# Kernel optimization log

Measured on AMD Instinct MI355X. Metric: run time of the kernel, lower is better.

Reference implementation:

```python
import jax, jax.numpy as jnp
import numpy as np

N_SUPPORT = 32768
N_QUERY = 16384
D = 512
K = 32
U = 128
NEG_BIG = -1e30  # masked-out attention logit; all-masked class -> uniform weights == mean fallback


def setup_inputs() -> dict:
    key = jax.random.key(0)
    k1, k2, k3, k4, k5 = jax.random.split(key, 5)
    query = jax.random.normal(k1, (N_QUERY, D), dtype=jnp.float32)
    support = jax.random.normal(k2, (N_SUPPORT, D), dtype=jnp.float32)
    labels = jax.random.randint(k3, (N_SUPPORT,), 0, K, dtype=jnp.int32)
    # Xavier-normal-ish init for per-class projection V (U,D) and attention vector w (U,1)
    V = jax.random.normal(k4, (K, U, D), dtype=jnp.float32) * np.float32(np.sqrt(2.0 / (U + D)))
    w = jax.random.normal(k5, (K, U), dtype=jnp.float32) * np.float32(np.sqrt(2.0 / (U + 1)))
    return {"query_embeddings": query, "support_embeddings": support,
            "support_labels": labels, "V": V, "w": w}


def reference(query_embeddings, support_embeddings, support_labels, V, w):
    # --- attention-weighted prototypes (vectorized over classes via masked softmax) ---
    # projected[k,n,u] = tanh(V[k] @ x_n)
    projected = jnp.tanh(jnp.einsum('nd,kud->knu', support_embeddings, V))
    attn_logits = jnp.einsum('knu,ku->kn', projected, w)              # (K, N)
    mask = support_labels[None, :] == jnp.arange(K, dtype=support_labels.dtype)[:, None]
    attn_logits = jnp.where(mask, attn_logits, NEG_BIG)
    # per-class softmax over support samples; an empty class yields uniform weights,
    # i.e. prototype = mean(embeddings) -- exactly the torch fallback branch.
    attn = jax.nn.softmax(attn_logits, axis=1)                        # (K, N)
    prototypes = jnp.einsum('kn,nd->kd', attn, support_embeddings)    # (K, D)

    # --- squared-euclidean distance classification ---
    q2 = jnp.sum(query_embeddings * query_embeddings, axis=1, keepdims=True)   # (B, 1)
    p2 = jnp.sum(prototypes * prototypes, axis=1)[None, :]                     # (1, K)
    dists = q2 + p2 - 2.0 * (query_embeddings @ prototypes.T)                  # (B, K)
    return jax.nn.log_softmax(-dists, axis=1)
```

## Files before the change

### kernel.cpp

```cpp
#include <hip/hip_runtime.h>
#include <hip/hip_bf16.h>

#define N_SUPPORT 32768
#define N_QUERY   16384
#define DIM       512
#define NCLS      32
#define NU        128
#define NBLK      (N_SUPPORT / 256)

#define OFF_IDX      0
#define OFF_COUNT    131072
#define OFF_START    131200
#define OFF_M        131456
#define OFF_Z        131584
#define OFF_P2       131712
#define OFF_LOGIT    132096
#define OFF_PRAW     263168
#define OFF_PROTO    328704
#define OFF_BHIST    394240
#define OFF_BOFFS    410624
#define OFF_VBF      458752
#define OFF_PBF      4653056

typedef __attribute__((ext_vector_type(8))) short short8;
typedef __attribute__((ext_vector_type(4))) short short4v;
typedef __attribute__((ext_vector_type(4))) float f32x4;

typedef __attribute__((address_space(3))) unsigned int lds_u32;
typedef const __attribute__((address_space(1))) unsigned int glb_u32;

__device__ inline unsigned short f2bf(float f) {
    unsigned int x = __builtin_bit_cast(unsigned int, f);
    unsigned int r = x + 0x7fffu + ((x >> 16) & 1u);
    return (unsigned short)(r >> 16);
}
__device__ inline float bf2f(unsigned short h) {
    unsigned int u = ((unsigned int)h) << 16;
    return __builtin_bit_cast(float, u);
}

__device__ inline short8 pack_bf8(float4 f0, float4 f1) {
    short8 pk;
    pk[0] = f2bf(f0.x); pk[1] = f2bf(f0.y); pk[2] = f2bf(f0.z); pk[3] = f2bf(f0.w);
    pk[4] = f2bf(f1.x); pk[5] = f2bf(f1.y); pk[6] = f2bf(f1.z); pk[7] = f2bf(f1.w);
    return pk;
}

__device__ inline void pack_hilo(float4 f0, float4 f1, short8& hi, short8& lo) {
    float v[8] = {f0.x, f0.y, f0.z, f0.w, f1.x, f1.y, f1.z, f1.w};
    #pragma unroll
    for (int i = 0; i < 8; i++) {
        unsigned short h = f2bf(v[i]);
        hi[i] = (short)h;
        lo[i] = (short)f2bf(v[i] - bf2f(h));
    }
}

__global__ void k_vcast(const float* __restrict__ V, short* __restrict__ Vbf,
                        float* __restrict__ praw, const int* __restrict__ labels,
                        int* __restrict__ bhist) {
    __shared__ int h[NCLS];
    int tid = threadIdx.x;
    bool dohist = (blockIdx.x < NBLK);
    if (dohist) {
        if (tid < NCLS) h[tid] = 0;
        __syncthreads();
        atomicAdd(&h[labels[blockIdx.x * 256 + tid]], 1);
    }
    int i = blockIdx.x * 256 + tid;
    int ob = i * 4;
    int j0  = ob & 7;
    int s   = (ob >> 3) & 7;
    int u   = (ob >> 6) & 127;
    int c   = (ob >> 13) & 7;
    int k   = ob >> 16;
    int d   = c * 64 + ((s ^ (u & 7)) * 8) + j0;
    float4 f = *(const float4*)(V + ((size_t)(k * 128 + u) * DIM + d));
    short4v o;
    o[0] = f2bf(f.x); o[1] = f2bf(f.y); o[2] = f2bf(f.z); o[3] = f2bf(f.w);
    *(short4v*)(Vbf + (size_t)ob) = o;
    if (i < (NCLS * DIM) / 4) *(float4*)(praw + i * 4) = make_float4(0.f, 0.f, 0.f, 0.f);
    if (dohist) {
        __syncthreads();
        if (tid < NCLS) bhist[blockIdx.x * NCLS + tid] = h[tid];
    }
}

__global__ void k_scan2(const int* __restrict__ bhist, int* __restrict__ boffs,
                        int* __restrict__ start, int* __restrict__ count) {
    __shared__ int tot[NCLS];
    int tid = threadIdx.x;
    if (tid < NCLS) {
        int s = 0;
        for (int b = 0; b < NBLK; b++) {
            boffs[b * NCLS + tid] = s;
            s += bhist[b * NCLS + tid];
        }
        tot[tid] = s;
    }
    __syncthreads();
    if (tid == 0) {
        int run = 0;
        for (int k = 0; k < NCLS; k++) {
            start[k] = run;
            count[k] = tot[k];
            run += tot[k];
        }
        start[NCLS] = run;
    }
}

__global__ void k_scatter(const int* __restrict__ labels, const int* __restrict__ boffs,
                          const int* __restrict__ start, int* __restrict__ idx_c) {
    __shared__ int whist[4][NCLS];
    int tid = threadIdx.x;
    int n = blockIdx.x * 256 + tid;
    int l = labels[n];
    int lane = tid & 63, wid = tid >> 6;
    unsigned long long mymask = 0ull;
    #pragma unroll
    for (int k = 0; k < NCLS; k++) {
        unsigned long long mk = __ballot(l == k);
        if (k == l) mymask = mk;
        if (lane == k) whist[wid][k] = __popcll(mk);
    }
    int rank = __popcll(mymask & ((1ull << lane) - 1ull));
    __syncthreads();
    int wbase = 0;
    for (int w = 0; w < wid; w++) wbase += whist[w][l];
    idx_c[start[l] + boffs[blockIdx.x * NCLS + l] + wbase + rank] = n;
}

__launch_bounds__(256, 1)
__global__ void k_logits(const float* __restrict__ support, const short* __restrict__ Vbf,
                         const float* __restrict__ w, const int* __restrict__ idx_c,
                         const int* __restrict__ start, const int* __restrict__ count,
                         float* __restrict__ logit_c) {
    int k = blockIdx.y;
    int cnt = count[k];
    int base = blockIdx.x * 32;
    if (base >= cnt) return;
    int M = min(32, cnt - base);
    int s0 = start[k] + base;
    int t = threadIdx.x;

    __shared__ __align__(16) short Xs[32 * 64];
    __shared__ __align__(16) short Vs[128 * 64];
    __shared__ float part[4][32];
    __shared__ int sidx[32];
    if (t < 32) sidx[t] = idx_c[s0 + ((t < M) ? t : 0)];
    __syncthreads();

    int l = t & 63, wv = t >> 6;
    int lo16 = l & 15, hi4 = l >> 4;

    int xrow = t >> 3, xslot = t & 7;
    int xdst = xrow * 64 + ((xslot ^ (xrow & 7)) * 8);
    const float* xsrc = support + (size_t)sidx[xrow] * DIM + xslot * 8;
    const short* Vkc = Vbf + (size_t)k * (8 * 128 * 64);

    f32x4 acc[2][2];
    #pragma unroll
    for (int mt = 0; mt < 2; mt++)
        #pragma unroll
        for (int nt = 0; nt < 2; nt++) acc[mt][nt] = (f32x4){0.f, 0.f, 0.f, 0.f};

    float4 xv0 = *(const float4*)(xsrc);
    float4 xv1 = *(const float4*)(xsrc + 4);

    for (int c = 0; c < 8; ++c) {
        __syncthreads();
        #pragma unroll
        for (int rep = 0; rep < 4; rep++) {
            int u = t + 256 * rep;
            __builtin_amdgcn_global_load_lds(
                (glb_u32*)(Vkc + (size_t)c * 8192 + (size_t)u * 8),
                (lds_u32*)&Vs[u * 8], 16, 0, 0);
        }
        *(short8*)&Xs[xdst] = pack_bf8(xv0, xv1);
        __syncthreads();
        if (c < 7) {
            xv0 = *(const float4*)(xsrc + (c + 1) * 64);
            xv1 = *(const float4*)(xsrc + (c + 1) * 64 + 4);
        }
        #pragma unroll
        for (int ks = 0; ks < 2; ks++) {
            short8 a[2], b[2];
            #pragma unroll
            for (int mt = 0; mt < 2; mt++) {
                int ar = mt * 16 + lo16;
                a[mt] = *(short8*)&Xs[ar * 64 + (((ks * 4 + hi4) ^ (ar & 7)) * 8)];
            }
            #pragma unroll
            for (int nt = 0; nt < 2; nt++) {
                int vr = wv * 32 + nt * 16 + lo16;
                b[nt] = *(short8*)&Vs[vr * 64 + (((ks * 4 + hi4) ^ (vr & 7)) * 8)];
            }
            #pragma unroll
            for (int mt = 0; mt < 2; mt++)
                #pragma unroll
                for (int nt = 0; nt < 2; nt++)
                    acc[mt][nt] = __builtin_amdgcn_mfma_f32_16x16x32_bf16(a[mt], b[nt], acc[mt][nt], 0, 0, 0);
        }
    }

    float w0 = w[k * NU + wv * 32 + lo16];
    float w1 = w[k * NU + wv * 32 + 16 + lo16];
    #pragma unroll
    for (int mt = 0; mt < 2; mt++) {
        #pragma unroll
        for (int r = 0; r < 4; r++) {
            float val = tanhf(acc[mt][0][r]) * w0 + tanhf(acc[mt][1][r]) * w1;
            val += __shfl_xor(val, 1);
            val += __shfl_xor(val, 2);
            val += __shfl_xor(val, 4);
            val += __shfl_xor(val, 8);
            if (lo16 == 0) part[wv][mt * 16 + hi4 * 4 + r] = val;
        }
    }
    __syncthreads();
    if (t < M) {
        logit_c[s0 + t] = part[0][t] + part[1][t] + part[2][t] + part[3][t];
    }
}

__global__ void k_mz(const float* __restrict__ logit_c, const int* __restrict__ start,
                     const int* __restrict__ count, float* __restrict__ m, float* __restrict__ Z) {
    int k = blockIdx.x;
    int cnt = count[k], s0 = start[k];
    int tid = threadIdx.x;
    __shared__ float red[256];
    float mx = -1e30f;
    for (int i = tid; i < cnt; i += 256) mx = fmaxf(mx, logit_c[s0 + i]);
    red[tid] = mx; __syncthreads();
    for (int off = 128; off > 0; off >>= 1) {
        if (tid < off) red[tid] = fmaxf(red[tid], red[tid + off]);
        __syncthreads();
    }
    float mk = red[0];
    __syncthreads();
    float s = 0.f;
    for (int i = tid; i < cnt; i += 256) s += expf(logit_c[s0 + i] - mk);
    red[tid] = s; __syncthreads();
    for (int off = 128; off > 0; off >>= 1) {
        if (tid < off) red[tid] += red[tid + off];
        __syncthreads();
    }
    if (tid == 0) { m[k] = mk; Z[k] = red[0]; }
}

__launch_bounds__(512, 1)
__global__ void k_proto(const float* __restrict__ support, const int* __restrict__ idx_c,
                        const float* __restrict__ logit_c, const int* __restrict__ start,
                        const int* __restrict__ count, const float* __restrict__ m,
                        float* __restrict__ praw) {
    int k = blockIdx.y;
    int cnt = count[k];
    int base = blockIdx.x * 64;
    if (base >= cnt) return;
    int M = min(64, cnt - base);
    int s0 = start[k] + base;
    __shared__ float wts[64];
    __shared__ int sid[64];
    int t = threadIdx.x;
    if (t < 64) {
        sid[t] = idx_c[s0 + ((t < M) ? t : 0)];
        wts[t] = (t < M) ? expf(logit_c[s0 + t] - m[k]) : 0.f;
    }
    __syncthreads();
    int d = t;
    float a = 0.f;
    for (int s = 0; s < 64; s += 4) {
        float r0 = support[(size_t)sid[s + 0] * DIM + d];
        float r1 = support[(size_t)sid[s + 1] * DIM + d];
        float r2 = support[(size_t)sid[s + 2] * DIM + d];
        float r3 = support[(size_t)sid[s + 3] * DIM + d];
        a += wts[s] * r0 + wts[s + 1] * r1 + wts[s + 2] * r2 + wts[s + 3] * r3;
    }
    atomicAdd(&praw[k * DIM + d], a);
}

__global__ void k_protonorm(const float* __restrict__ support, const float* __restrict__ praw,
                            const float* __restrict__ Z, const int* __restrict__ count,
                            float* __restrict__ proto, float* __restrict__ p2,
                            short* __restrict__ Pbf) {
    int k = blockIdx.x;
    int tid = threadIdx.x;
    int cnt = count[k];
    __shared__ float red[256];
    float pv[2];
    if (cnt > 0) {
        float inv = 1.f / Z[k];
        #pragma unroll
        for (int i = 0; i < 2; i++) pv[i] = praw[k * DIM + tid + i * 256] * inv;
    } else {
        #pragma unroll
        for (int i = 0; i < 2; i++) {
            int d = tid + i * 256;
            float s = 0.f;
            for (int n = 0; n < N_SUPPORT; n++) s += support[(size_t)n * DIM + d];
            pv[i] = s * (1.f / N_SUPPORT);
        }
    }
    float acc = 0.f;
    #pragma unroll
    for (int i = 0; i < 2; i++) {
        int d = tid + i * 256;
        proto[k * DIM + d] = pv[i];
        acc += pv[i] * pv[i];
        int c = d >> 6, off = d & 63, o = off >> 3, j = off & 7;
        int s = o ^ (k & 7);
        int pos = (c * 32 + k) * 64 + s * 8 + j;
        unsigned short hi = f2bf(pv[i]);
        Pbf[pos] = (short)hi;
        Pbf[NCLS * DIM + pos] = (short)f2bf(pv[i] - bf2f(hi));
    }
    red[tid] = acc; __syncthreads();
    for (int off = 128; off > 0; off >>= 1) {
        if (tid < off) red[tid] += red[tid + off];
        __syncthreads();
    }
    if (tid == 0) p2[k] = red[0];
}

__launch_bounds__(256, 1)
__global__ void k_dist(const float* __restrict__ query, const short* __restrict__ Pbf,
                       const float* __restrict__ p2, float* __restrict__ out) {
    __shared__ __align__(16) short Ph[NCLS * DIM];
    __shared__ __align__(16) short Pl[NCLS * DIM];
    __shared__ __align__(16) short Qh[2][64 * 64];
    __shared__ __align__(16) short Ql[2][64 * 64];
    int t = threadIdx.x;
    int qbase = blockIdx.x * 64;
    int l = t & 63, wv = t >> 6;
    int lo16 = l & 15, hi4 = l >> 4;

    #pragma unroll
    for (int rep = 0; rep < 8; rep++) {
        int u = t + 256 * rep;
        ((short8*)Ph)[u] = ((const short8*)Pbf)[u];
        ((short8*)Pl)[u] = ((const short8*)(Pbf + NCLS * DIM))[u];
    }

    int qrow[2], qslot[2], qdst[2];
    const float* qsrc[2];
    #pragma unroll
    for (int rep = 0; rep < 2; rep++) {
        int u = t + 256 * rep;
        qrow[rep] = u >> 3; qslot[rep] = u & 7;
        qdst[rep] = qrow[rep] * 64 + ((qslot[rep] ^ (qrow[rep] & 7)) * 8);
        qsrc[rep] = query + (size_t)(qbase + qrow[rep]) * DIM + qslot[rep] * 8;
    }

    f32x4 acc[2];
    acc[0] = (f32x4){0.f, 0.f, 0.f, 0.f};
    acc[1] = (f32x4){0.f, 0.f, 0.f, 0.f};

    float4 qa[2][2], qb[2][2];
#define LOADQ(d, c) { _Pragma("unroll") for (int rep = 0; rep < 2; rep++) { \
        d[rep][0] = *(const float4*)(qsrc[rep] + (c) * 64);                 \
        d[rep][1] = *(const float4*)(qsrc[rep] + (c) * 64 + 4); } }
#define WRITEQ(buf, d) { _Pragma("unroll") for (int rep = 0; rep < 2; rep++) { \
        short8 hi8, lo8;                                                        \
        pack_hilo(d[rep][0], d[rep][1], hi8, lo8);                              \
        *(short8*)&Qh[buf][qdst[rep]] = hi8;                                    \
        *(short8*)&Ql[buf][qdst[rep]] = lo8; } }

    LOADQ(qa, 0);
    LOADQ(qb, 1);
    WRITEQ(0, qa);

    for (int c = 0; c < 8; ++c) {
        int cur = c & 1;
        __syncthreads();
        if (c + 2 < 8) {
            if (cur == 0) { LOADQ(qa, c + 2); }
            else          { LOADQ(qb, c + 2); }
        }
        #pragma unroll
        for (int ks = 0; ks < 2; ks++) {
            int arow = wv * 16 + lo16;
            int asw = ((ks * 4 + hi4) ^ (arow & 7)) * 8;
            short8 ah = *(short8*)&Qh[cur][arow * 64 + asw];
            short8 al = *(short8*)&Ql[cur][arow * 64 + asw];
            #pragma unroll
            for (int nt = 0; nt < 2; nt++) {
                int brow = nt * 16 + lo16;
                int pos = (c * 32 + brow) * 64 + (((ks * 4 + hi4) ^ (brow & 7)) * 8);
                short8 bh = *(short8*)&Ph[pos];
                short8 bl = *(short8*)&Pl[pos];
                acc[nt] = __builtin_amdgcn_mfma_f32_16x16x32_bf16(ah, bh, acc[nt], 0, 0, 0);
                acc[nt] = __builtin_amdgcn_mfma_f32_16x16x32_bf16(ah, bl, acc[nt], 0, 0, 0);
                acc[nt] = __builtin_amdgcn_mfma_f32_16x16x32_bf16(al, bh, acc[nt], 0, 0, 0);
            }
        }
        if (c < 7) {
            if (cur == 0) { WRITEQ(1, qb); }
            else          { WRITEQ(0, qa); }
        }
    }
#undef LOADQ
#undef WRITEQ

    float p2v0 = p2[lo16];
    float p2v1 = p2[16 + lo16];
    #pragma unroll
    for (int r = 0; r < 4; r++) {
        float l0 = 2.f * acc[0][r] - p2v0;
        float l1 = 2.f * acc[1][r] - p2v1;
        float mx = fmaxf(l0, l1);
        mx = fmaxf(mx, __shfl_xor(mx, 1));
        mx = fmaxf(mx, __shfl_xor(mx, 2));
        mx = fmaxf(mx, __shfl_xor(mx, 4));
        mx = fmaxf(mx, __shfl_xor(mx, 8));
        float s = expf(l0 - mx) + expf(l1 - mx);
        s += __shfl_xor(s, 1);
        s += __shfl_xor(s, 2);
        s += __shfl_xor(s, 4);
        s += __shfl_xor(s, 8);
        float lse = mx + logf(s);
        int q = qbase + wv * 16 + hi4 * 4 + r;
        out[(size_t)q * NCLS + lo16] = l0 - lse;
        out[(size_t)q * NCLS + 16 + lo16] = l1 - lse;
    }
}

extern "C" void kernel_launch(void* const* d_in, const int* in_sizes, int n_in,
                              void* d_out, int out_size, void* d_ws, size_t ws_size,
                              hipStream_t stream) {
    const float* query   = (const float*)d_in[0];
    const float* support = (const float*)d_in[1];
    const int*   labels  = (const int*)d_in[2];
    const float* V       = (const float*)d_in[3];
    const float* w       = (const float*)d_in[4];
    float* out = (float*)d_out;
    char* ws = (char*)d_ws;

    int*   idx_c   = (int*)(ws + OFF_IDX);
    int*   count   = (int*)(ws + OFF_COUNT);
    int*   start   = (int*)(ws + OFF_START);
    float* m       = (float*)(ws + OFF_M);
    float* Z       = (float*)(ws + OFF_Z);
    float* p2      = (float*)(ws + OFF_P2);
    float* logit_c = (float*)(ws + OFF_LOGIT);
    float* praw    = (float*)(ws + OFF_PRAW);
    float* proto   = (float*)(ws + OFF_PROTO);
    int*   bhist   = (int*)(ws + OFF_BHIST);
    int*   boffs   = (int*)(ws + OFF_BOFFS);
    short* vbf     = (short*)(ws + OFF_VBF);
    short* pbf     = (short*)(ws + OFF_PBF);

    hipLaunchKernelGGL(k_vcast, dim3((NCLS * NU * DIM) / 1024), dim3(256), 0, stream,
                       V, vbf, praw, labels, bhist);
    hipLaunchKernelGGL(k_scan2, dim3(1), dim3(64), 0, stream, bhist, boffs, start, count);
    hipLaunchKernelGGL(k_scatter, dim3(NBLK), dim3(256), 0, stream, labels, boffs, start, idx_c);
    hipLaunchKernelGGL(k_logits, dim3(64, NCLS), dim3(256), 0, stream,
                       support, vbf, w, idx_c, start, count, logit_c);
    hipLaunchKernelGGL(k_mz, dim3(NCLS), dim3(256), 0, stream, logit_c, start, count, m, Z);
    hipLaunchKernelGGL(k_proto, dim3(32, NCLS), dim3(512), 0, stream,
                       support, idx_c, logit_c, start, count, m, praw);
    hipLaunchKernelGGL(k_protonorm, dim3(NCLS), dim3(256), 0, stream,
                       support, praw, Z, count, proto, p2, pbf);
    hipLaunchKernelGGL(k_dist, dim3(N_QUERY / 64), dim3(256), 0, stream, query, pbf, p2, out);
}
```

Before: 73.50 us.

## Load V fragments directly into registers and stage full X tile once

The logits kernel stops streaming V through LDS in eight synchronized chunks. Each wave now reads its own V B-fragments straight from global memory into registers, in two halves of four chunks each. The whole 32x512 bf16 X tile is gathered and written to swizzled LDS up front, so only one barrier is needed. This removes seven per-chunk barrier pairs and the LDS round trip for V, at the cost of many more live registers (32 short8 V fragments plus 16 float4 X values) and a larger X shared buffer.

```diff
diff --git a/kernel.cpp b/kernel.cpp
--- a/kernel.cpp
+++ b/kernel.cpp
@@ -25,9 +25,6 @@
 typedef __attribute__((ext_vector_type(8))) short short8;
 typedef __attribute__((ext_vector_type(4))) short short4v;
 typedef __attribute__((ext_vector_type(4))) float f32x4;
-
-typedef __attribute__((address_space(3))) unsigned int lds_u32;
-typedef const __attribute__((address_space(1))) unsigned int glb_u32;
 
 __device__ inline unsigned short f2bf(float f) {
     unsigned int x = __builtin_bit_cast(unsigned int, f);
@@ -144,65 +141,82 @@
     int s0 = start[k] + base;
     int t = threadIdx.x;
 
-    __shared__ __align__(16) short Xs[32 * 64];
-    __shared__ __align__(16) short Vs[128 * 64];
+    __shared__ __align__(16) short Xs[32 * 512];
     __shared__ float part[4][32];
-    __shared__ int sidx[32];
-    if (t < 32) sidx[t] = idx_c[s0 + ((t < M) ? t : 0)];
-    __syncthreads();
 
     int l = t & 63, wv = t >> 6;
     int lo16 = l & 15, hi4 = l >> 4;
 
-    int xrow = t >> 3, xslot = t & 7;
-    int xdst = xrow * 64 + ((xslot ^ (xrow & 7)) * 8);
-    const float* xsrc = support + (size_t)sidx[xrow] * DIM + xslot * 8;
-    const short* Vkc = Vbf + (size_t)k * (8 * 128 * 64);
-
-    f32x4 acc[2][2];
-    #pragma unroll
-    for (int mt = 0; mt < 2; mt++)
-        #pragma unroll
-        for (int nt = 0; nt < 2; nt++) acc[mt][nt] = (f32x4){0.f, 0.f, 0.f, 0.f};
-
-    float4 xv0 = *(const float4*)(xsrc);
-    float4 xv1 = *(const float4*)(xsrc + 4);
-
-    for (int c = 0; c < 8; ++c) {
-        __syncthreads();
-        #pragma unroll
-        for (int rep = 0; rep < 4; rep++) {
-            int u = t + 256 * rep;
-            __builtin_amdgcn_global_load_lds(
-                (glb_u32*)(Vkc + (size_t)c * 8192 + (size_t)u * 8),
-                (lds_u32*)&Vs[u * 8], 16, 0, 0);
-        }
-        *(short8*)&Xs[xdst] = pack_bf8(xv0, xv1);
-        __syncthreads();
-        if (c < 7) {
-            xv0 = *(const float4*)(xsrc + (c + 1) * 64);
-            xv1 = *(const float4*)(xsrc + (c + 1) * 64 + 4);
-        }
-        #pragma unroll
-        for (int ks = 0; ks < 2; ks++) {
-            short8 a[2], b[2];
-            #pragma unroll
-            for (int mt = 0; mt < 2; mt++) {
-                int ar = mt * 16 + lo16;
-                a[mt] = *(short8*)&Xs[ar * 64 + (((ks * 4 + hi4) ^ (ar & 7)) * 8)];
-            }
+    float4 xf[8][2];
+    #pragma unroll
+    for (int rep = 0; rep < 8; rep++) {
+        int row = wv + 4 * rep;
+        int r = (row < M) ? row : 0;
+        int nidx = idx_c[s0 + r];
+        const float* src = support + (size_t)nidx * DIM + l * 8;
+        xf[rep][0] = *(const float4*)src;
+        xf[rep][1] = *(const float4*)(src + 4);
+    }
+
+    const short* Vk = Vbf + (size_t)k * (8 * 128 * 64);
+    short8 vreg[4][2][2];
+    #pragma unroll
+    for (int c = 0; c < 4; c++)
+        #pragma unroll
+        for (int ks = 0; ks < 2; ks++)
             #pragma unroll
             for (int nt = 0; nt < 2; nt++) {
-                int vr = wv * 32 + nt * 16 + lo16;
-                b[nt] = *(short8*)&Vs[vr * 64 + (((ks * 4 + hi4) ^ (vr & 7)) * 8)];
+                int u = wv * 32 + nt * 16 + lo16;
+                int q = ks * 4 + hi4;
+                vreg[c][ks][nt] = *(const short8*)(Vk + (size_t)c * 8192 + (size_t)u * 64 + ((q ^ (u & 7)) * 8));
             }
+
+    #pragma unroll
+    for (int rep = 0; rep < 8; rep++) {
+        int row = wv + 4 * rep;
+        *(short8*)&Xs[row * 512 + ((l ^ (row & 7)) * 8)] = pack_bf8(xf[rep][0], xf[rep][1]);
+    }
+
+    f32x4 acc[2][2];
+    #pragma unroll
+    for (int mt = 0; mt < 2; mt++)
+        #pragma unroll
+        for (int nt = 0; nt < 2; nt++) acc[mt][nt] = (f32x4){0.f, 0.f, 0.f, 0.f};
+
+    __syncthreads();
+
+#define COMPUTE(c, vb) { _Pragma("unroll")                                        \
+    for (int ks = 0; ks < 2; ks++) {                                              \
+        short8 a[2];                                                              \
+        _Pragma("unroll")                                                         \
+        for (int mt = 0; mt < 2; mt++) {                                          \
+            int ar = mt * 16 + lo16;                                              \
+            int cu = (c) * 8 + ks * 4 + hi4;                                      \
+            a[mt] = *(short8*)&Xs[ar * 512 + ((cu ^ (ar & 7)) * 8)];              \
+        }                                                                         \
+        _Pragma("unroll")                                                         \
+        for (int mt = 0; mt < 2; mt++)                                            \
+            _Pragma("unroll")                                                     \
+            for (int nt = 0; nt < 2; nt++)                                        \
+                acc[mt][nt] = __builtin_amdgcn_mfma_f32_16x16x32_bf16(a[mt], vb[ks][nt], acc[mt][nt], 0, 0, 0); \
+    } }
+
+    #pragma unroll
+    for (int c = 0; c < 4; c++) COMPUTE(c, vreg[c]);
+
+    #pragma unroll
+    for (int c = 0; c < 4; c++)
+        #pragma unroll
+        for (int ks = 0; ks < 2; ks++)
             #pragma unroll
-            for (int mt = 0; mt < 2; mt++)
-                #pragma unroll
-                for (int nt = 0; nt < 2; nt++)
-                    acc[mt][nt] = __builtin_amdgcn_mfma_f32_16x16x32_bf16(a[mt], b[nt], acc[mt][nt], 0, 0, 0);
-        }
-    }
+            for (int nt = 0; nt < 2; nt++) {
+                int u = wv * 32 + nt * 16 + lo16;
+                int q = ks * 4 + hi4;
+                vreg[c][ks][nt] = *(const short8*)(Vk + (size_t)(c + 4) * 8192 + (size_t)u * 64 + ((q ^ (u & 7)) * 8));
+            }
+    #pragma unroll
+    for (int c = 0; c < 4; c++) COMPUTE(c + 4, vreg[c]);
+#undef COMPUTE
 
     float w0 = w[k * NU + wv * 32 + lo16];
     float w1 = w[k * NU + wv * 32 + 16 + lo16];
```

Result: no change. 72.08 us (-1.9%).
